# Performance work log

Measured on AMD Instinct MI355X. Metric: run time of the kernel, lower is better.

## Reference

```python
import jax, jax.numpy as jnp
import numpy as np

ALIGNED_H, ALIGNED_W, ALIGNED_T = 7, 7, 4
SPATIAL_SCALE, TIME_SCALE = 1.0 / 16.0, 1.0
B, C, T, H, W = 4, 256, 16, 64, 64
N_ROIS = 1200


def setup_inputs() -> dict:
    key = jax.random.key(0)
    kf, kb, kx, ky, kw, kh, kt, kd = jax.random.split(key, 8)
    features = jax.random.normal(kf, (B, C, T, H, W), dtype=jnp.float32)
    b = jax.random.randint(kb, (N_ROIS,), 0, B).astype(jnp.float32)
    # image-space boxes (1024x1024 image, stride-16 features); temporal interval in frame units
    x1 = jax.random.uniform(kx, (N_ROIS,), minval=0.0, maxval=700.0)
    y1 = jax.random.uniform(ky, (N_ROIS,), minval=0.0, maxval=700.0)
    x2 = jnp.minimum(x1 + jax.random.uniform(kw, (N_ROIS,), minval=32.0, maxval=320.0), 1023.0)
    y2 = jnp.minimum(y1 + jax.random.uniform(kh, (N_ROIS,), minval=32.0, maxval=320.0), 1023.0)
    t1 = jax.random.uniform(kt, (N_ROIS,), minval=0.0, maxval=10.0)
    t2 = jnp.minimum(t1 + jax.random.uniform(kd, (N_ROIS,), minval=2.0, maxval=6.0), 15.0)
    rois = jnp.stack([b, x1, y1, x2, y2, t1, t2], axis=1)  # [N, 7]
    return {"features": features, "rois": rois}


def _axis_samples(start, end, size, n_out):
    # classic roi_align sampling: bin = (end - start + 1) / (n_out - 1), sample at start + i*bin
    length = jnp.maximum(end - start + 1.0, 1.0)                                  # [N]
    step = length / (n_out - 1.0)
    coord = start[:, None] + step[:, None] * jnp.arange(n_out, dtype=jnp.float32)[None, :]  # [N, n_out]
    valid = (coord >= 0.0) & (coord < size)
    lo = jnp.clip(jnp.floor(coord), 0.0, size - 1.0)
    frac = coord - lo
    lo_i = lo.astype(jnp.int32)
    hi_i = jnp.minimum(lo_i + 1, size - 1)
    return lo_i, hi_i, frac, valid.astype(jnp.float32)


def roi_align_3d(features, rois, p_t, p_h, p_w, sscale, tscale):
    Bf, Cf, Tf, Hf, Wf = features.shape
    f = jnp.transpose(features, (0, 2, 3, 4, 1))  # [B,T,H,W,C] channel-last for clean gather
    bidx = rois[:, 0].astype(jnp.int32)
    x1 = rois[:, 1] * sscale
    y1 = rois[:, 2] * sscale
    x2 = rois[:, 3] * sscale
    y2 = rois[:, 4] * sscale
    t1 = rois[:, 5] * tscale
    t2 = rois[:, 6] * tscale
    tl, th, tfr, tv = _axis_samples(t1, t2, Tf, p_t)  # [N, p_t]
    yl, yh, yfr, yv = _axis_samples(y1, y2, Hf, p_h)  # [N, p_h]
    xl, xh, xfr, xv = _axis_samples(x1, x2, Wf, p_w)  # [N, p_w]
    b4 = bidx[:, None, None, None]
    out = jnp.zeros((rois.shape[0], p_t, p_h, p_w, Cf), dtype=features.dtype)
    # trilinear interpolation: sum over 8 corners
    for ti, wt in ((tl, 1.0 - tfr), (th, tfr)):
        for yi, wy in ((yl, 1.0 - yfr), (yh, yfr)):
            for xi, wx in ((xl, 1.0 - xfr), (xh, xfr)):
                v = f[b4, ti[:, :, None, None], yi[:, None, :, None], xi[:, None, None, :]]  # [N,pt,ph,pw,C]
                w = wt[:, :, None, None] * wy[:, None, :, None] * wx[:, None, None, :]
                out = out + v * w[..., None]
    # zero out-of-bounds sample points (matches CUDA kernel behavior)
    mask = tv[:, :, None, None] * yv[:, None, :, None] * xv[:, None, None, :]
    out = out * mask[..., None]
    return jnp.transpose(out, (0, 4, 1, 2, 3))  # [N, C, p_t, p_h, p_w]


def _avg_pool3d_k2s1(x):
    s = x[..., :-1, :, :] + x[..., 1:, :, :]
    s = s[..., :, :-1, :] + s[..., :, 1:, :]
    s = s[..., :, :, :-1] + s[..., :, :, 1:]
    return s * 0.125


def reference(features, rois):
    x = roi_align_3d(features, rois, ALIGNED_T + 1, ALIGNED_H + 1, ALIGNED_W + 1,
                     SPATIAL_SCALE, TIME_SCALE)
    return _avg_pool3d_k2s1(x)  # [N, C, ALIGNED_T, ALIGNED_H, ALIGNED_W]
```

## Files before the change

kernel.cpp:

```cpp
#include <hip/hip_runtime.h>

#define C_ 256
#define T_ 16
#define H_ 64
#define W_ 64
#define PT 5
#define PH 8
#define PW 8
#define OT 4
#define OH 7
#define OW 7
#define SSCALE (1.0f/16.0f)
#define TSCALE 1.0f
#define CG 64
#define LROW 66
#define PLN (CG * LROW)
#define NOUT (CG * OT * OH * OW)

typedef float f4v __attribute__((ext_vector_type(4)));
typedef float f2v __attribute__((ext_vector_type(2)));
typedef _Float16 h2v __attribute__((ext_vector_type(2)));
typedef _Float16 h8v __attribute__((ext_vector_type(8)));

__device__ __forceinline__ f4v lo4(h8v h) {
    f4v r = {(float)h[0], (float)h[1], (float)h[2], (float)h[3]};
    return r;
}
__device__ __forceinline__ f4v hi4(h8v h) {
    f4v r = {(float)h[4], (float)h[5], (float)h[6], (float)h[7]};
    return r;
}

__global__ __launch_bounds__(256) void transpose_kernel(const float* __restrict__ f,
                                                        _Float16* __restrict__ ft) {
    __shared__ unsigned tile[64 * 128];
    const int THW = T_ * H_ * W_;
    int thw0 = blockIdx.x * 64;
    int b = blockIdx.y;
    int q = threadIdx.x & 15;
    int cp0 = threadIdx.x >> 4;

#pragma unroll
    for (int k = 0; k < 8; ++k) {
        int cp = k * 16 + cp0;
        int c = cp * 2;
        const f4v* s0 = reinterpret_cast<const f4v*>(
            &f[((size_t)b * C_ + c) * THW + thw0 + q * 4]);
        const f4v* s1 = reinterpret_cast<const f4v*>(
            &f[((size_t)b * C_ + c + 1) * THW + thw0 + q * 4]);
        f4v va = __builtin_nontemporal_load(s0);
        f4v vb = __builtin_nontemporal_load(s1);
#pragma unroll
        for (int j = 0; j < 4; ++j) {
            int row = q * 4 + j;
            h2v hp = {(_Float16)va[j], (_Float16)vb[j]};
            tile[row * 128 + (cp ^ (row & 30))] = __builtin_bit_cast(unsigned, hp);
        }
    }
    __syncthreads();

    int wv = threadIdx.x >> 6;
    int ln = threadIdx.x & 63;
    size_t orow = ((size_t)b * THW + thw0) * C_;
#pragma unroll
    for (int i = 0; i < 16; ++i) {
        int row = wv * 16 + i;
        int s = row & 30;
        uint2 w = *reinterpret_cast<const uint2*>(&tile[row * 128 + ((ln * 2) ^ s)]);
        *reinterpret_cast<uint2*>(&ft[orow + (size_t)row * C_ + ln * 4]) = w;
    }
}

__global__ __launch_bounds__(1024) void sort_rois(const float* __restrict__ rois,
                                                  int nroi, int* __restrict__ perm) {
    __shared__ unsigned key[2048];
    int t = threadIdx.x;
    if (nroi > 2048) {
        for (int i = t; i < nroi; i += 1024) perm[i] = i;
        return;
    }
    for (int i = t; i < 2048; i += 1024) {
        unsigned k = 0x1FFFFFu;
        if (i < nroi) {
            const float* rp = rois + i * 7;
            int bb = (int)rp[0];
            float xc = (rp[1] + rp[3]) * 0.5f * SSCALE;
            float yc = (rp[2] + rp[4]) * 0.5f * SSCALE;
            float tc = (rp[5] + rp[6]) * 0.5f * TSCALE;
            int xq = min(63, max(0, (int)xc));
            int yq = min(63, max(0, (int)yc));
            int tq = min(15, max(0, (int)tc));
            unsigned m = 0;
#pragma unroll
            for (int bit = 0; bit < 6; ++bit)
                m |= (((yq >> bit) & 1u) << (2 * bit + 1)) |
                     (((xq >> bit) & 1u) << (2 * bit));
            k = ((((unsigned)bb << 12) | m) << 4) | (unsigned)tq;
        }
        key[i] = (k << 11) | (unsigned)i;
    }
    __syncthreads();
    for (int kk = 2; kk <= 2048; kk <<= 1) {
        for (int j = kk >> 1; j > 0; j >>= 1) {
            for (int i = t; i < 2048; i += 1024) {
                int ixj = i ^ j;
                if (ixj > i) {
                    unsigned a = key[i], c = key[ixj];
                    bool up = (i & kk) == 0;
                    if ((a > c) == up) { key[i] = c; key[ixj] = a; }
                }
            }
            __syncthreads();
        }
    }
    for (int i = t; i < 2048; i += 1024)
        if (i < nroi) perm[i] = (int)(key[i] & 0x7FFu);
}

__global__ __launch_bounds__(512) void roi_kernel(const _Float16* __restrict__ ft,
                                                  const float* __restrict__ rois,
                                                  const int* __restrict__ perm,
                                                  float* __restrict__ out) {
    __shared__ float scratch[NOUT];
    __shared__ float sroi[7];
    __shared__ int2 s_trow[PT]; __shared__ float2 s_twt[PT];
    __shared__ int2 s_yrow[PH]; __shared__ float2 s_ywt[PH];
    __shared__ int2 s_xoff[PW]; __shared__ float2 s_xwt[PW];

    int bid = blockIdx.x;
    int r = perm[bid >> 2];
    int cg = bid & 3;
    int c0 = cg * CG;

    if (threadIdx.x < 7) sroi[threadIdx.x] = rois[r * 7 + threadIdx.x];
    __syncthreads();

    if (threadIdx.x < 21) {
        int i = threadIdx.x;
        float start, end, size;
        int j, n, scale;
        if (i < 5) {
            j = i; n = PT;
            start = sroi[5] * TSCALE; end = sroi[6] * TSCALE;
            size = (float)T_; scale = H_ * W_ * C_ * 2;
        } else if (i < 13) {
            j = i - 5; n = PH;
            start = sroi[2] * SSCALE; end = sroi[4] * SSCALE;
            size = (float)H_; scale = W_ * C_ * 2;
        } else {
            j = i - 13; n = PW;
            start = sroi[1] * SSCALE; end = sroi[3] * SSCALE;
            size = (float)W_; scale = C_ * 2;
        }
        float length = fmaxf(end - start + 1.0f, 1.0f);
        float step = length / (float)(n - 1);
        float coord = start + step * (float)j;
        float valid = (coord >= 0.0f && coord < size) ? 1.0f : 0.0f;
        float lo = fminf(fmaxf(floorf(coord), 0.0f), size - 1.0f);
        int lo_i = (int)lo;
        int hi_i = min(lo_i + 1, (int)size - 1);
        float fr = coord - lo;
        int2 offs; offs.x = lo_i * scale; offs.y = hi_i * scale;
        float2 wts; wts.x = (1.0f - fr) * valid; wts.y = fr * valid;
        if (i < 5)       { s_trow[j] = offs; s_twt[j] = wts; }
        else if (i < 13) { s_yrow[j] = offs; s_ywt[j] = wts; }
        else             { s_xoff[j] = offs; s_xwt[j] = wts; }
    }
    __syncthreads();

    int b = (int)sroi[0];
    int c8 = threadIdx.x & 7;
    int slot = threadIdx.x >> 3;
    const char* fb = (const char*)ft
        + ((size_t)b * (T_ * H_ * W_ * C_) + (size_t)(c0 + c8 * 8)) * 2;

    float* bufs[2] = {scratch, scratch + PLN};
    int cc = threadIdx.x & 63;
    int hh = threadIdx.x >> 6;

    float racc[OT][OW];
#pragma unroll
    for (int t = 0; t < OT; ++t)
#pragma unroll
        for (int w = 0; w < OW; ++w) racc[t][w] = 0.0f;

    int y = slot >> 3, x = slot & 7;
    int2 yr = s_yrow[y]; float2 yw = s_ywt[y];
    int2 xo = s_xoff[x]; float2 xw = s_xwt[x];
    int o00 = yr.x + xo.x, o01 = yr.x + xo.y;
    int o10 = yr.y + xo.x, o11 = yr.y + xo.y;

    int ia = -1, ib = -1;
    f4v aL, aH, bL, bH;
    aL = aH = bL = bH = (f4v){0.f, 0.f, 0.f, 0.f};

#pragma unroll
    for (int t = 0; t < PT; ++t) {
        int2 trv = s_trow[t];
        int trx = __builtin_amdgcn_readfirstlane(trv.x);
        int trY = __builtin_amdgcn_readfirstlane(trv.y);
        float2 tw = s_twt[t];

        if (ia != trx) {
            if (ib == trx) { aL = bL; aH = bH; ia = trx; }
            else {
                h8v q00 = *(const h8v*)(fb + trx + o00);
                h8v q01 = *(const h8v*)(fb + trx + o01);
                h8v q10 = *(const h8v*)(fb + trx + o10);
                h8v q11 = *(const h8v*)(fb + trx + o11);
                aL = yw.x * (xw.x * lo4(q00) + xw.y * lo4(q01))
                   + yw.y * (xw.x * lo4(q10) + xw.y * lo4(q11));
                aH = yw.x * (xw.x * hi4(q00) + xw.y * hi4(q01))
                   + yw.y * (xw.x * hi4(q10) + xw.y * hi4(q11));
                ia = trx;
            }
        }
        if (ib != trY) {
            if (ia == trY) { bL = aL; bH = aH; ib = trY; }
            else {
                h8v p00 = *(const h8v*)(fb + trY + o00);
                h8v p01 = *(const h8v*)(fb + trY + o01);
                h8v p10 = *(const h8v*)(fb + trY + o10);
                h8v p11 = *(const h8v*)(fb + trY + o11);
                bL = yw.x * (xw.x * lo4(p00) + xw.y * lo4(p01))
                   + yw.y * (xw.x * lo4(p10) + xw.y * lo4(p11));
                bH = yw.x * (xw.x * hi4(p00) + xw.y * hi4(p01))
                   + yw.y * (xw.x * hi4(p10) + xw.y * hi4(p11));
                ib = trY;
            }
        }

        f4v vL = tw.x * aL + tw.y * bL;
        f4v vH = tw.x * aH + tw.y * bH;

        float* bp = bufs[t & 1];
        {
            float* col = &bp[(c8 * 8) * LROW + slot];
            col[0 * LROW] = vL[0];
            col[1 * LROW] = vL[1];
            col[2 * LROW] = vL[2];
            col[3 * LROW] = vL[3];
            col[4 * LROW] = vH[0];
            col[5 * LROW] = vH[1];
            col[6 * LROW] = vH[2];
            col[7 * LROW] = vH[3];
        }
        __syncthreads();

        if (hh < 7) {
            const float* p = &bp[cc * LROW + hh * 8];
            float p2[8];
#pragma unroll
            for (int x2 = 0; x2 < 4; ++x2) {
                f2v a = *(const f2v*)(p + 2 * x2);
                f2v bq = *(const f2v*)(p + 8 + 2 * x2);
                f2v s = a + bq;
                p2[2 * x2] = s[0];
                p2[2 * x2 + 1] = s[1];
            }
#pragma unroll
            for (int w = 0; w < OW; ++w) {
                float pw = p2[w] + p2[w + 1];
                if (t < OT) racc[t][w] += pw;
                if (t > 0) racc[t - 1][w] += pw;
            }
        }
    }
    __syncthreads();

    if (hh < 7) {
        int base = cc * (OT * OH * OW) + hh * OW;
#pragma unroll
        for (int t = 0; t < OT; ++t)
#pragma unroll
            for (int w = 0; w < OW; ++w)
                scratch[base + t * (OH * OW) + w] = racc[t][w] * 0.125f;
    }
    __syncthreads();

    float* outb = out + ((size_t)r * C_ + c0) * (OT * OH * OW);
    const f4v* s4 = (const f4v*)scratch;
    f4v* o4 = (f4v*)outb;
#pragma unroll
    for (int k = 0; k < 7; ++k) {
        int idx = k * 512 + threadIdx.x;
        if (idx < NOUT / 4) __builtin_nontemporal_store(s4[idx], &o4[idx]);
    }
}

__device__ __forceinline__ void axis_sample(float start, float end, float size, int n,
                                            int j, int& lo_i, int& hi_i, float& frac,
                                            float& valid) {
    float length = fmaxf(end - start + 1.0f, 1.0f);
    float step = length / (float)(n - 1);
    float coord = start + step * (float)j;
    valid = (coord >= 0.0f && coord < size) ? 1.0f : 0.0f;
    float lo = fminf(fmaxf(floorf(coord), 0.0f), size - 1.0f);
    frac = coord - lo;
    lo_i = (int)lo;
    hi_i = min(lo_i + 1, (int)size - 1);
}

__global__ void roi_direct(const float* __restrict__ f, const float* __restrict__ rois,
                           float* __restrict__ out, long long total) {
    long long idx = (long long)blockIdx.x * 256 + threadIdx.x;
    if (idx >= total) return;
    int w = (int)(idx % OW);
    long long q = idx / OW;
    int h = (int)(q % OH);
    q /= OH;
    int t = (int)(q % OT);
    q /= OT;
    int c = (int)(q % C_);
    int r = (int)(q / C_);

    float rb = rois[r * 7 + 0];
    float x1 = rois[r * 7 + 1] * SSCALE;
    float y1 = rois[r * 7 + 2] * SSCALE;
    float x2 = rois[r * 7 + 3] * SSCALE;
    float y2 = rois[r * 7 + 4] * SSCALE;
    float t1 = rois[r * 7 + 5] * TSCALE;
    float t2 = rois[r * 7 + 6] * TSCALE;
    int b = (int)rb;
    const float* fc = f + ((size_t)b * C_ + c) * (T_ * H_ * W_);

    float acc = 0.0f;
    for (int dt = 0; dt < 2; ++dt) {
        int tlo, thi; float tf, tv;
        axis_sample(t1, t2, (float)T_, PT, t + dt, tlo, thi, tf, tv);
        for (int dh = 0; dh < 2; ++dh) {
            int ylo, yhi; float yf, yv;
            axis_sample(y1, y2, (float)H_, PH, h + dh, ylo, yhi, yf, yv);
            for (int dw = 0; dw < 2; ++dw) {
                int xlo, xhi; float xf, xv;
                axis_sample(x1, x2, (float)W_, PW, w + dw, xlo, xhi, xf, xv);
                float v000 = fc[(tlo * H_ + ylo) * W_ + xlo];
                float v001 = fc[(tlo * H_ + ylo) * W_ + xhi];
                float v010 = fc[(tlo * H_ + yhi) * W_ + xlo];
                float v011 = fc[(tlo * H_ + yhi) * W_ + xhi];
                float v100 = fc[(thi * H_ + ylo) * W_ + xlo];
                float v101 = fc[(thi * H_ + ylo) * W_ + xhi];
                float v110 = fc[(thi * H_ + yhi) * W_ + xlo];
                float v111 = fc[(thi * H_ + yhi) * W_ + xhi];
                float vx00 = v000 + xf * (v001 - v000);
                float vx01 = v010 + xf * (v011 - v010);
                float vx10 = v100 + xf * (v101 - v100);
                float vx11 = v110 + xf * (v111 - v110);
                float vy0 = vx00 + yf * (vx01 - vx00);
                float vy1 = vx10 + yf * (vx11 - vx10);
                float v = vy0 + tf * (vy1 - vy0);
                acc += v * (tv * yv * xv);
            }
        }
    }
    out[idx] = acc * 0.125f;
}

extern "C" void kernel_launch(void* const* d_in, const int* in_sizes, int n_in,
                              void* d_out, int out_size, void* d_ws, size_t ws_size,
                              hipStream_t stream) {
    const float* feat = (const float*)d_in[0];
    const float* rois = (const float*)d_in[1];
    float* out = (float*)d_out;
    int nroi = in_sizes[1] / 7;
    int B = in_sizes[0] / (C_ * T_ * H_ * W_);
    size_t ftbytes = (size_t)B * T_ * H_ * W_ * C_ * sizeof(_Float16);
    size_t need = ftbytes + 2048 * sizeof(int);

    if (ws_size >= need && nroi >= 1) {
        _Float16* ft = (_Float16*)d_ws;
        int* perm = (int*)((char*)d_ws + ftbytes);
        sort_rois<<<1, 1024, 0, stream>>>(rois, nroi, perm);
        dim3 g1(T_ * H_ * W_ / 64, B);
        transpose_kernel<<<g1, 256, 0, stream>>>(feat, ft);
        roi_kernel<<<dim3(nroi * (C_ / CG)), 512, 0, stream>>>(ft, rois, perm, out);
    } else {
        long long total = (long long)nroi * C_ * OT * OH * OW;
        roi_direct<<<(int)((total + 255) / 256), 256, 0, stream>>>(feat, rois, out, total);
    }
}
```

Before: 514.9 us.

## Fuse ROI sort into transpose launch and shrink roi_kernel shared memory

The single-block ROI sort moves into an extra block of the transpose kernel, which removes one kernel launch. That block sorts with 256 threads instead of 1024, so its bitonic sort takes more steps and may now be the last block to finish. The roi_kernel output staging buffer is cut from the full 64x196 output to two plane-sized halves, written out in two temporal passes. Together with launch_bounds(512,8), this is meant to raise occupancy, at the cost of an extra barrier round and 8-byte stores with index division instead of 16-byte nontemporal stores.

```diff
diff --git a/kernel.cpp b/kernel.cpp
--- a/kernel.cpp
+++ b/kernel.cpp
@@ -32,9 +32,59 @@
 }
 
 __global__ __launch_bounds__(256) void transpose_kernel(const float* __restrict__ f,
-                                                        _Float16* __restrict__ ft) {
+                                                        _Float16* __restrict__ ft,
+                                                        const float* __restrict__ rois,
+                                                        int nroi, int* __restrict__ perm) {
     __shared__ unsigned tile[64 * 128];
     const int THW = T_ * H_ * W_;
+
+    if (blockIdx.x == gridDim.x - 1) {
+        if (blockIdx.y != 0) return;
+        unsigned* key = tile;
+        int t = threadIdx.x;
+        if (nroi > 2048) {
+            for (int i = t; i < nroi; i += 256) perm[i] = i;
+            return;
+        }
+        for (int i = t; i < 2048; i += 256) {
+            unsigned k = 0x1FFFFFu;
+            if (i < nroi) {
+                const float* rp = rois + i * 7;
+                int bb = (int)rp[0];
+                float xc = (rp[1] + rp[3]) * 0.5f * SSCALE;
+                float yc = (rp[2] + rp[4]) * 0.5f * SSCALE;
+                float tc = (rp[5] + rp[6]) * 0.5f * TSCALE;
+                int xq = min(63, max(0, (int)xc));
+                int yq = min(63, max(0, (int)yc));
+                int tq = min(15, max(0, (int)tc));
+                unsigned m = 0;
+#pragma unroll
+                for (int bit = 0; bit < 6; ++bit)
+                    m |= (((yq >> bit) & 1u) << (2 * bit + 1)) |
+                         (((xq >> bit) & 1u) << (2 * bit));
+                k = ((((unsigned)bb << 12) | m) << 4) | (unsigned)tq;
+            }
+            key[i] = (k << 11) | (unsigned)i;
+        }
+        __syncthreads();
+        for (int kk = 2; kk <= 2048; kk <<= 1) {
+            for (int j = kk >> 1; j > 0; j >>= 1) {
+                for (int i = t; i < 2048; i += 256) {
+                    int ixj = i ^ j;
+                    if (ixj > i) {
+                        unsigned a = key[i], c = key[ixj];
+                        bool up = (i & kk) == 0;
+                        if ((a > c) == up) { key[i] = c; key[ixj] = a; }
+                    }
+                }
+                __syncthreads();
+            }
+        }
+        for (int i = t; i < 2048; i += 256)
+            if (i < nroi) perm[i] = (int)(key[i] & 0x7FFu);
+        return;
+    }
+
     int thw0 = blockIdx.x * 64;
     int b = blockIdx.y;
     int q = threadIdx.x & 15;
@@ -71,57 +121,11 @@
     }
 }
 
-__global__ __launch_bounds__(1024) void sort_rois(const float* __restrict__ rois,
-                                                  int nroi, int* __restrict__ perm) {
-    __shared__ unsigned key[2048];
-    int t = threadIdx.x;
-    if (nroi > 2048) {
-        for (int i = t; i < nroi; i += 1024) perm[i] = i;
-        return;
-    }
-    for (int i = t; i < 2048; i += 1024) {
-        unsigned k = 0x1FFFFFu;
-        if (i < nroi) {
-            const float* rp = rois + i * 7;
-            int bb = (int)rp[0];
-            float xc = (rp[1] + rp[3]) * 0.5f * SSCALE;
-            float yc = (rp[2] + rp[4]) * 0.5f * SSCALE;
-            float tc = (rp[5] + rp[6]) * 0.5f * TSCALE;
-            int xq = min(63, max(0, (int)xc));
-            int yq = min(63, max(0, (int)yc));
-            int tq = min(15, max(0, (int)tc));
-            unsigned m = 0;
-#pragma unroll
-            for (int bit = 0; bit < 6; ++bit)
-                m |= (((yq >> bit) & 1u) << (2 * bit + 1)) |
-                     (((xq >> bit) & 1u) << (2 * bit));
-            k = ((((unsigned)bb << 12) | m) << 4) | (unsigned)tq;
-        }
-        key[i] = (k << 11) | (unsigned)i;
-    }
-    __syncthreads();
-    for (int kk = 2; kk <= 2048; kk <<= 1) {
-        for (int j = kk >> 1; j > 0; j >>= 1) {
-            for (int i = t; i < 2048; i += 1024) {
-                int ixj = i ^ j;
-                if (ixj > i) {
-                    unsigned a = key[i], c = key[ixj];
-                    bool up = (i & kk) == 0;
-                    if ((a > c) == up) { key[i] = c; key[ixj] = a; }
-                }
-            }
-            __syncthreads();
-        }
-    }
-    for (int i = t; i < 2048; i += 1024)
-        if (i < nroi) perm[i] = (int)(key[i] & 0x7FFu);
-}
-
-__global__ __launch_bounds__(512) void roi_kernel(const _Float16* __restrict__ ft,
-                                                  const float* __restrict__ rois,
-                                                  const int* __restrict__ perm,
-                                                  float* __restrict__ out) {
-    __shared__ float scratch[NOUT];
+__global__ __launch_bounds__(512, 8) void roi_kernel(const _Float16* __restrict__ ft,
+                                                     const float* __restrict__ rois,
+                                                     const int* __restrict__ perm,
+                                                     float* __restrict__ out) {
+    __shared__ float scratch[2 * PLN];
     __shared__ float sroi[7];
     __shared__ int2 s_trow[PT]; __shared__ float2 s_twt[PT];
     __shared__ int2 s_yrow[PH]; __shared__ float2 s_ywt[PH];
@@ -268,23 +272,31 @@
     }
     __syncthreads();
 
-    if (hh < 7) {
-        int base = cc * (OT * OH * OW) + hh * OW;
-#pragma unroll
-        for (int t = 0; t < OT; ++t)
-#pragma unroll
-            for (int w = 0; w < OW; ++w)
-                scratch[base + t * (OH * OW) + w] = racc[t][w] * 0.125f;
-    }
-    __syncthreads();
-
     float* outb = out + ((size_t)r * C_ + c0) * (OT * OH * OW);
-    const f4v* s4 = (const f4v*)scratch;
-    f4v* o4 = (f4v*)outb;
-#pragma unroll
-    for (int k = 0; k < 7; ++k) {
-        int idx = k * 512 + threadIdx.x;
-        if (idx < NOUT / 4) __builtin_nontemporal_store(s4[idx], &o4[idx]);
+#pragma unroll
+    for (int tp = 0; tp < 2; ++tp) {
+        if (hh < 7) {
+            int base = cc * 98 + hh * 7;
+#pragma unroll
+            for (int tt = 0; tt < 2; ++tt)
+#pragma unroll
+                for (int w = 0; w < OW; ++w)
+                    scratch[base + tt * 49 + w] = racc[2 * tp + tt][w] * 0.125f;
+        }
+        __syncthreads();
+        {
+            const f2v* s2 = (const f2v*)scratch;
+            f2v* o2 = (f2v*)(outb + tp * 98);
+            for (int k = 0; k < 7; ++k) {
+                int j = k * 512 + (int)threadIdx.x;
+                if (j < 3136) {
+                    int c = j / 49;
+                    int qf = j - c * 49;
+                    o2[c * 98 + qf] = s2[j];
+                }
+            }
+        }
+        if (tp == 0) __syncthreads();
     }
 }
 
@@ -370,9 +382,8 @@
     if (ws_size >= need && nroi >= 1) {
         _Float16* ft = (_Float16*)d_ws;
         int* perm = (int*)((char*)d_ws + ftbytes);
-        sort_rois<<<1, 1024, 0, stream>>>(rois, nroi, perm);
-        dim3 g1(T_ * H_ * W_ / 64, B);
-        transpose_kernel<<<g1, 256, 0, stream>>>(feat, ft);
+        dim3 g1(T_ * H_ * W_ / 64 + 1, B);
+        transpose_kernel<<<g1, 256, 0, stream>>>(feat, ft, rois, nroi, perm);
         roi_kernel<<<dim3(nroi * (C_ / CG)), 512, 0, stream>>>(ft, rois, perm, out);
     } else {
         long long total = (long long)nroi * C_ * OT * OH * OW;
```

After: 681.8 us. 32.4% more time.
